# Optimization experiments

Measured on AMD Instinct MI355X. Metric: run time of the kernel, lower is better.

## Reference

```python
import jax, jax.numpy as jnp
import numpy as np
import math

C = 128

def setup_inputs() -> dict:
    key = jax.random.key(0)
    ks = jax.random.split(key, 6)
    B, N, M = 4, 8192, 2048
    s = 1.0 / math.sqrt(C)
    return {
        "pcd_up": jax.random.normal(ks[0], (B, C, N), dtype=jnp.float32),
        "pcd_down": jax.random.normal(ks[1], (B, C, M), dtype=jnp.float32),
        "wq": jax.random.normal(ks[2], (C, C), dtype=jnp.float32) * s,
        "wk": jax.random.normal(ks[3], (C, C), dtype=jnp.float32) * s,
        "wv": jax.random.normal(ks[4], (C, C), dtype=jnp.float32) * s,
        "wskip": jax.random.normal(ks[5], (C, C), dtype=jnp.float32) * s,
    }

def reference(pcd_up, pcd_down, wq, wk, wv, wskip):
    # Conv1d(kernel=1, no bias) == per-point linear: w @ x over channel dim
    q = jnp.einsum('oc,bcn->bon', wq, pcd_up)      # [B,C,N]
    k = jnp.einsum('oc,bcm->bom', wk, pcd_down)    # [B,C,M]
    v = jnp.einsum('oc,bcm->bom', wv, pcd_down)    # [B,C,M]
    energy = jnp.einsum('bcn,bcm->bnm', q, k)      # [B,N,M]
    scale = math.sqrt(q.shape[1])                  # sqrt(C): q.shape[-2] in torch
    attn = jax.nn.softmax(energy / scale, axis=-1)
    x = jnp.einsum('bnm,bcm->bcn', attn, v)        # [B,C,N]
    skip = jnp.einsum('oc,bcn->bon', wskip, pcd_up)
    return skip + x
```

## Files before the change

### kernel.cpp

```cpp
#include <hip/hip_runtime.h>
#include <hip/hip_bf16.h>
#include <math.h>

#define C_DIM 128
#define B_DIM 4
#define N_DIM 8192
#define M_DIM 2048
#define NT_KV 32

typedef unsigned short u16;
typedef unsigned int u32;
typedef short bf16x8 __attribute__((ext_vector_type(8)));
typedef float f32x4 __attribute__((ext_vector_type(4)));
typedef float f32x16 __attribute__((ext_vector_type(16)));
typedef u32 u32x4 __attribute__((ext_vector_type(4)));

__device__ inline u16 f2bf(float f) {
  u32 u = __builtin_bit_cast(u32, f);
  u += 0x7fffu + ((u >> 16) & 1u);
  return (u16)(u >> 16);
}
__device__ inline u32 cvtpk_bf16(float lo, float hi) {
  u32 r;
  asm("v_cvt_pk_bf16_f32 %0, %1, %2" : "=v"(r) : "v"(lo), "v"(hi));
  return r;
}

template <int MODE>
__device__ inline void proj_pass(const float* __restrict__ W, float wscale,
                                 const u16* __restrict__ xt_s,
                                 u16* __restrict__ outh,
                                 int b, int X, int x0, int t) {
  const int l = t & 63, w = t >> 6, lr = l & 15, lh = (l >> 4) & 3;
  bf16x8 wf[2][4];
  #pragma unroll
  for (int ot = 0; ot < 2; ++ot)
    #pragma unroll
    for (int kc = 0; kc < 4; ++kc) {
      const float* wp = &W[(size_t)(w * 32 + ot * 16 + lr) * 128 + kc * 32 + lh * 8];
      float4 a0 = *(const float4*)wp;
      float4 a1 = *(const float4*)(wp + 4);
      bf16x8 f;
      f[0] = (short)f2bf(a0.x * wscale); f[1] = (short)f2bf(a0.y * wscale);
      f[2] = (short)f2bf(a0.z * wscale); f[3] = (short)f2bf(a0.w * wscale);
      f[4] = (short)f2bf(a1.x * wscale); f[5] = (short)f2bf(a1.y * wscale);
      f[6] = (short)f2bf(a1.z * wscale); f[7] = (short)f2bf(a1.w * wscale);
      wf[ot][kc] = f;
    }
  f32x4 acc[2][4];
  #pragma unroll
  for (int ot = 0; ot < 2; ++ot)
    #pragma unroll
    for (int xt = 0; xt < 4; ++xt) acc[ot][xt] = 0.f;

  #pragma unroll
  for (int xt = 0; xt < 4; ++xt) {
    int xx = xt * 16 + lr;
    #pragma unroll
    for (int kc = 0; kc < 4; ++kc) {
      bf16x8 bf = *(const bf16x8*)&xt_s[xx * 128 + ((kc * 32 + lh * 8) ^ ((xx & 15) << 3))];
      #pragma unroll
      for (int ot = 0; ot < 2; ++ot)
        acc[ot][xt] = __builtin_amdgcn_mfma_f32_16x16x32_bf16(wf[ot][kc], bf, acc[ot][xt], 0, 0, 0);
    }
  }
  #pragma unroll
  for (int ot = 0; ot < 2; ++ot) {
    int o0 = w * 32 + ot * 16 + lh * 4;
    #pragma unroll
    for (int xt = 0; xt < 4; ++xt) {
      int xg = x0 + xt * 16 + lr;
      if constexpr (MODE == 0) {
        u16 h[4];
        #pragma unroll
        for (int r = 0; r < 4; ++r) h[r] = f2bf(acc[ot][xt][r]);
        *(uint2*)&outh[((size_t)b * X + xg) * 128 + o0] = *(uint2*)h;
      } else if constexpr (MODE == 2) {
        int tt = xg >> 6, mt = (xg >> 5) & 1, ms = xg & 31;
        int kcK = o0 >> 4, lh1p = (o0 >> 3) & 1, e0 = o0 & 7;
        u16 h[4];
        #pragma unroll
        for (int r = 0; r < 4; ++r) h[r] = f2bf(acc[ot][xt][r]);
        size_t off = ((((size_t)(b * NT_KV + tt) * 2 + mt) * 8 + kcK) * 64 + (ms | (lh1p << 5))) * 8 + e0;
        *(uint2*)&outh[off] = *(uint2*)h;
      } else {
        int tt = xg >> 6, sv = (xg >> 4) & 3, lh1m = (xg >> 3) & 1, e = xg & 7;
        int ctv = o0 >> 5;
        #pragma unroll
        for (int r = 0; r < 4; ++r) {
          int cs = (o0 + r) & 31;
          size_t off = ((((size_t)(b * NT_KV + tt) * 4 + ctv) * 4 + sv) * 64 + (cs | (lh1m << 5))) * 8 + e;
          outh[off] = f2bf(acc[ot][xt][r]);
        }
      }
    }
  }
}

__global__ __launch_bounds__(256, 2) void proj_all(
    const float* __restrict__ up, const float* __restrict__ down,
    const float* __restrict__ wq, const float* __restrict__ wk,
    const float* __restrict__ wv, u16* __restrict__ Qt,
    u16* __restrict__ Kt2, u16* __restrict__ Vp, float qscale) {
  __shared__ u16 xt_s[64 * 128];
  const int bid = blockIdx.x, t = threadIdx.x;
  const bool isQ = bid < 512;
  const int sub = isQ ? bid : bid - 512;
  const int b = sub & 3;
  const int x0 = (sub >> 2) * 64;
  const int X = isQ ? N_DIM : M_DIM;
  const float* in = isQ ? up : down;

  #pragma unroll
  for (int pp = 0; pp < 8; ++pp) {
    int c = pp * 16 + (t >> 4);
    int x4 = (t & 15) * 4;
    float4 v = *(const float4*)&in[((size_t)b * 128 + c) * X + x0 + x4];
    xt_s[(x4 + 0) * 128 + (c ^ (((x4 + 0) & 15) << 3))] = f2bf(v.x);
    xt_s[(x4 + 1) * 128 + (c ^ (((x4 + 1) & 15) << 3))] = f2bf(v.y);
    xt_s[(x4 + 2) * 128 + (c ^ (((x4 + 2) & 15) << 3))] = f2bf(v.z);
    xt_s[(x4 + 3) * 128 + (c ^ (((x4 + 3) & 15) << 3))] = f2bf(v.w);
  }
  __syncthreads();
  if (isQ) {
    proj_pass<0>(wq, qscale, xt_s, Qt, b, X, x0, t);
  } else {
    proj_pass<2>(wk, 1.0f, xt_s, Kt2, b, X, x0, t);
    proj_pass<3>(wv, 1.0f, xt_s, Vp, b, X, x0, t);
  }
}

__device__ inline void stage_kv(const u16* __restrict__ gK, const u16* __restrict__ gV,
                                u16* lK, u16* lV, int tile, int t) {
  const u16* ks = gK + (size_t)tile * 8192;
  const u16* vs = gV + (size_t)tile * 8192;
  #pragma unroll
  for (int i = 0; i < 2; ++i) {
    int ch = t + i * 512;
    __builtin_amdgcn_global_load_lds((const __attribute__((address_space(1))) void*)(ks + ch * 8),
                                     (__attribute__((address_space(3))) void*)(lK + ch * 8), 16, 0, 0);
    __builtin_amdgcn_global_load_lds((const __attribute__((address_space(1))) void*)(vs + ch * 8),
                                     (__attribute__((address_space(3))) void*)(lV + ch * 8), 16, 0, 0);
  }
}

__global__ __launch_bounds__(512, 2) void attn_kernel(
    const u16* __restrict__ Qt, const u16* __restrict__ Kt2,
    const u16* __restrict__ Vp, const float* __restrict__ up,
    const float* __restrict__ wskip, float* __restrict__ out) {
  __shared__ union {
    u16 kv[2][2][8192];
    float od[4][4096];
  } lds;
  __shared__ float lb[4][64];

  const int bid = blockIdx.x;
  const int xcd = bid & 7, b = xcd & 3, slot = bid >> 3;
  const int n0 = ((xcd >> 2) * 32 + slot) * 128;
  const int t = threadIdx.x, w = t >> 6, l = t & 63, lh1 = l >> 5;
  const int h = w >> 2;
  const int nq = n0 + (w & 3) * 32 + (l & 31);

  bf16x8 qf[8];
  #pragma unroll
  for (int kc = 0; kc < 8; ++kc)
    qf[kc] = *(const bf16x8*)&Qt[((size_t)b * N_DIM + nq) * 128 + kc * 16 + lh1 * 8];

  const u16* gK = Kt2 + (size_t)b * 262144;
  const u16* gV = Vp + (size_t)b * 262144;

  f32x16 acco[4];
  #pragma unroll
  for (int ct = 0; ct < 4; ++ct) acco[ct] = 0.f;
  float lrun = 0.f;

  bf16x8 pf[2];
  bf16x8 vreg[8];
  #pragma unroll
  for (int u = 0; u < 2; ++u) pf[u] = (bf16x8)0;
  #pragma unroll
  for (int x = 0; x < 8; ++x) vreg[x] = (bf16x8)0;

  stage_kv(gK, gV, lds.kv[0][0], lds.kv[0][1], 0, t);
  __syncthreads();

  #pragma unroll 2
  for (int i = 0; i < NT_KV; ++i) {
    const int cur = i & 1;
    if (i + 1 < NT_KV)
      stage_kv(gK, gV, lds.kv[cur ^ 1][0], lds.kv[cur ^ 1][1], i + 1, t);
    const u16* kl = lds.kv[cur][0];
    const u16* vl = lds.kv[cur][1];

    f32x16 sacc = 0.f;
    __builtin_amdgcn_s_setprio(1);
    #pragma unroll
    for (int kc = 0; kc < 8; ++kc) {
      bf16x8 kf = *(const bf16x8*)&kl[((h * 8 + kc) * 64 + l) * 8];
      sacc = __builtin_amdgcn_mfma_f32_32x32x16_bf16(kf, qf[kc], sacc, 0, 0, 0);
    }
    #pragma unroll
    for (int u = 0; u < 2; ++u)
      #pragma unroll
      for (int ct = 0; ct < 4; ++ct)
        acco[ct] = __builtin_amdgcn_mfma_f32_32x32x16_bf16(vreg[ct * 2 + u], pf[u], acco[ct], 0, 0, 0);
    __builtin_amdgcn_s_setprio(0);
    __builtin_amdgcn_sched_barrier(0);

    #pragma unroll
    for (int ct = 0; ct < 4; ++ct)
      #pragma unroll
      for (int u = 0; u < 2; ++u)
        vreg[ct * 2 + u] = *(const bf16x8*)&vl[((ct * 4 + 2 * h + u) * 64 + l) * 8];

    #pragma unroll
    for (int r = 0; r < 16; ++r) sacc[r] = exp2f(sacc[r]);
    {
      float a0 = (sacc[0] + sacc[1]) + (sacc[2] + sacc[3]);
      float a1 = (sacc[4] + sacc[5]) + (sacc[6] + sacc[7]);
      float a2 = (sacc[8] + sacc[9]) + (sacc[10] + sacc[11]);
      float a3 = (sacc[12] + sacc[13]) + (sacc[14] + sacc[15]);
      lrun += (a0 + a1) + (a2 + a3);
    }
    u32 gp[4][2];
    #pragma unroll
    for (int j = 0; j < 4; ++j) {
      gp[j][0] = cvtpk_bf16(sacc[j * 4 + 0], sacc[j * 4 + 1]);
      gp[j][1] = cvtpk_bf16(sacc[j * 4 + 2], sacc[j * 4 + 3]);
    }
    #pragma unroll
    for (int u = 0; u < 2; ++u) {
      u32 a0 = gp[2 * u][0], a1 = gp[2 * u][1];
      u32 b0 = gp[2 * u + 1][0], b1 = gp[2 * u + 1][1];
      asm("v_permlane32_swap_b32 %0, %1" : "+v"(a0), "+v"(b0));
      asm("v_permlane32_swap_b32 %0, %1" : "+v"(a1), "+v"(b1));
      u32x4 fv; fv.x = a0; fv.y = a1; fv.z = b0; fv.w = b1;
      pf[u] = __builtin_bit_cast(bf16x8, fv);
    }
    __syncthreads();
  }

  __builtin_amdgcn_s_setprio(1);
  #pragma unroll
  for (int u = 0; u < 2; ++u)
    #pragma unroll
    for (int ct = 0; ct < 4; ++ct)
      acco[ct] = __builtin_amdgcn_mfma_f32_32x32x16_bf16(vreg[ct * 2 + u], pf[u], acco[ct], 0, 0, 0);
  __builtin_amdgcn_s_setprio(0);

  float lt = lrun + __shfl_xor(lrun, 32, 64);

  if (w >= 4) {
    float* dst = lds.od[w - 4];
    #pragma unroll
    for (int ct = 0; ct < 4; ++ct)
      #pragma unroll
      for (int r = 0; r < 16; ++r) dst[(ct * 16 + r) * 64 + l] = acco[ct][r];
    lb[w - 4][l] = lt;
  }
  __syncthreads();
  if (w < 4) {
    const float* src = lds.od[w];
    #pragma unroll
    for (int ct = 0; ct < 4; ++ct)
      #pragma unroll
      for (int r = 0; r < 16; ++r) acco[ct][r] += src[(ct * 16 + r) * 64 + l];
    lt += lb[w][l];

    float inv = 1.0f / lt;
    #pragma unroll
    for (int ct = 0; ct < 4; ++ct)
      #pragma unroll
      for (int r = 0; r < 16; ++r) acco[ct][r] *= inv;

    const float* upb = up + (size_t)b * 128 * N_DIM;
    #pragma unroll
    for (int kc = 0; kc < 8; ++kc) {
      float uv[8];
      #pragma unroll
      for (int e = 0; e < 8; ++e)
        uv[e] = upb[(size_t)(kc * 16 + lh1 * 8 + e) * N_DIM + nq];
      u32x4 ufv;
      ufv.x = cvtpk_bf16(uv[0], uv[1]);
      ufv.y = cvtpk_bf16(uv[2], uv[3]);
      ufv.z = cvtpk_bf16(uv[4], uv[5]);
      ufv.w = cvtpk_bf16(uv[6], uv[7]);
      bf16x8 upf = __builtin_bit_cast(bf16x8, ufv);
      #pragma unroll
      for (int ct = 0; ct < 4; ++ct) {
        const float* wp = &wskip[(size_t)(ct * 32 + (l & 31)) * 128 + kc * 16 + lh1 * 8];
        float4 w0 = *(const float4*)wp;
        float4 w1 = *(const float4*)(wp + 4);
        u32x4 wfv;
        wfv.x = cvtpk_bf16(w0.x, w0.y);
        wfv.y = cvtpk_bf16(w0.z, w0.w);
        wfv.z = cvtpk_bf16(w1.x, w1.y);
        wfv.w = cvtpk_bf16(w1.z, w1.w);
        bf16x8 wsf = __builtin_bit_cast(bf16x8, wfv);
        acco[ct] = __builtin_amdgcn_mfma_f32_32x32x16_bf16(wsf, upf, acco[ct], 0, 0, 0);
      }
    }

    #pragma unroll
    for (int ct = 0; ct < 4; ++ct)
      #pragma unroll
      for (int r = 0; r < 16; ++r) {
        int c = ct * 32 + (r & 3) + 8 * (r >> 2) + 4 * lh1;
        out[((size_t)b * 128 + c) * N_DIM + nq] = acco[ct][r];
      }
  }
}

extern "C" void kernel_launch(void* const* d_in, const int* in_sizes, int n_in,
                              void* d_out, int out_size, void* d_ws, size_t ws_size,
                              hipStream_t stream) {
  const float* up    = (const float*)d_in[0];
  const float* down  = (const float*)d_in[1];
  const float* wq    = (const float*)d_in[2];
  const float* wk    = (const float*)d_in[3];
  const float* wv    = (const float*)d_in[4];
  const float* wskip = (const float*)d_in[5];
  float* out = (float*)d_out;

  u16* Qt  = (u16*)d_ws;
  u16* Kt2 = Qt + (size_t)B_DIM * N_DIM * C_DIM;
  u16* Vp  = Kt2 + (size_t)B_DIM * M_DIM * C_DIM;

  const float qscale = (float)(1.4426950408889634 / sqrt(128.0));

  hipLaunchKernelGGL((proj_all), dim3(640), dim3(256), 0, stream,
                     up, down, wq, wk, wv, Qt, Kt2, Vp, qscale);
  hipLaunchKernelGGL((attn_kernel), dim3(256), dim3(512), 0, stream,
                     Qt, Kt2, Vp, up, wskip, out);
}
```

Baseline: 70.34 us.

## Software-pipeline softmax of previous tile behind current QK MFMA

Restructures the KV loop so the QK^T MFMAs of tile i are issued first, then the exp2/sum/bf16-pack softmax of tile i-1 runs while those MFMAs are in flight, followed by the PV MFMAs. Two score accumulators (sA/sB) alternate, with a peeled prologue and epilogue. The goal is to overlap VALU exponentials with matrix-core work inside each wave. The cost is higher register pressure from the extra f32x16 accumulator, which could lower occupancy or cause spills.

After: 70.70 us. About the same (+0.5%).

```diff
diff --git a/kernel.cpp b/kernel.cpp
--- a/kernel.cpp
+++ b/kernel.cpp
@@ -176,29 +176,52 @@
 
   bf16x8 pf[2];
   bf16x8 vreg[8];
-  #pragma unroll
-  for (int u = 0; u < 2; ++u) pf[u] = (bf16x8)0;
-  #pragma unroll
-  for (int x = 0; x < 8; ++x) vreg[x] = (bf16x8)0;
-
-  stage_kv(gK, gV, lds.kv[0][0], lds.kv[0][1], 0, t);
-  __syncthreads();
-
-  #pragma unroll 2
-  for (int i = 0; i < NT_KV; ++i) {
+  f32x16 sA, sB;
+
+  auto do_sm = [&](f32x16& sp) {
+    #pragma unroll
+    for (int r = 0; r < 16; ++r) sp[r] = exp2f(sp[r]);
+    float a0 = (sp[0] + sp[1]) + (sp[2] + sp[3]);
+    float a1 = (sp[4] + sp[5]) + (sp[6] + sp[7]);
+    float a2 = (sp[8] + sp[9]) + (sp[10] + sp[11]);
+    float a3 = (sp[12] + sp[13]) + (sp[14] + sp[15]);
+    lrun += (a0 + a1) + (a2 + a3);
+    u32 gp[4][2];
+    #pragma unroll
+    for (int j = 0; j < 4; ++j) {
+      gp[j][0] = cvtpk_bf16(sp[j * 4 + 0], sp[j * 4 + 1]);
+      gp[j][1] = cvtpk_bf16(sp[j * 4 + 2], sp[j * 4 + 3]);
+    }
+    #pragma unroll
+    for (int u = 0; u < 2; ++u) {
+      u32 a0_ = gp[2 * u][0], a1_ = gp[2 * u][1];
+      u32 b0_ = gp[2 * u + 1][0], b1_ = gp[2 * u + 1][1];
+      asm("v_permlane32_swap_b32 %0, %1" : "+v"(a0_), "+v"(b0_));
+      asm("v_permlane32_swap_b32 %0, %1" : "+v"(a1_), "+v"(b1_));
+      u32x4 fv; fv.x = a0_; fv.y = a1_; fv.z = b0_; fv.w = b1_;
+      pf[u] = __builtin_bit_cast(bf16x8, fv);
+    }
+  };
+
+  auto body = [&](int i, f32x16& sc, f32x16& sp) {
     const int cur = i & 1;
     if (i + 1 < NT_KV)
       stage_kv(gK, gV, lds.kv[cur ^ 1][0], lds.kv[cur ^ 1][1], i + 1, t);
     const u16* kl = lds.kv[cur][0];
     const u16* vl = lds.kv[cur][1];
 
-    f32x16 sacc = 0.f;
+    sc = 0.f;
     __builtin_amdgcn_s_setprio(1);
     #pragma unroll
     for (int kc = 0; kc < 8; ++kc) {
       bf16x8 kf = *(const bf16x8*)&kl[((h * 8 + kc) * 64 + l) * 8];
-      sacc = __builtin_amdgcn_mfma_f32_32x32x16_bf16(kf, qf[kc], sacc, 0, 0, 0);
-    }
+      sc = __builtin_amdgcn_mfma_f32_32x32x16_bf16(kf, qf[kc], sc, 0, 0, 0);
+    }
+    __builtin_amdgcn_s_setprio(0);
+
+    do_sm(sp);
+
+    __builtin_amdgcn_s_setprio(1);
     #pragma unroll
     for (int u = 0; u < 2; ++u)
       #pragma unroll
@@ -213,33 +236,39 @@
       for (int u = 0; u < 2; ++u)
         vreg[ct * 2 + u] = *(const bf16x8*)&vl[((ct * 4 + 2 * h + u) * 64 + l) * 8];
 
-    #pragma unroll
-    for (int r = 0; r < 16; ++r) sacc[r] = exp2f(sacc[r]);
-    {
-      float a0 = (sacc[0] + sacc[1]) + (sacc[2] + sacc[3]);
-      float a1 = (sacc[4] + sacc[5]) + (sacc[6] + sacc[7]);
-      float a2 = (sacc[8] + sacc[9]) + (sacc[10] + sacc[11]);
-      float a3 = (sacc[12] + sacc[13]) + (sacc[14] + sacc[15]);
-      lrun += (a0 + a1) + (a2 + a3);
-    }
-    u32 gp[4][2];
-    #pragma unroll
-    for (int j = 0; j < 4; ++j) {
-      gp[j][0] = cvtpk_bf16(sacc[j * 4 + 0], sacc[j * 4 + 1]);
-      gp[j][1] = cvtpk_bf16(sacc[j * 4 + 2], sacc[j * 4 + 3]);
-    }
-    #pragma unroll
-    for (int u = 0; u < 2; ++u) {
-      u32 a0 = gp[2 * u][0], a1 = gp[2 * u][1];
-      u32 b0 = gp[2 * u + 1][0], b1 = gp[2 * u + 1][1];
-      asm("v_permlane32_swap_b32 %0, %1" : "+v"(a0), "+v"(b0));
-      asm("v_permlane32_swap_b32 %0, %1" : "+v"(a1), "+v"(b1));
-      u32x4 fv; fv.x = a0; fv.y = a1; fv.z = b0; fv.w = b1;
-      pf[u] = __builtin_bit_cast(bf16x8, fv);
-    }
     __syncthreads();
-  }
-
+  };
+
+  stage_kv(gK, gV, lds.kv[0][0], lds.kv[0][1], 0, t);
+  __syncthreads();
+
+  {
+    stage_kv(gK, gV, lds.kv[1][0], lds.kv[1][1], 1, t);
+    const u16* kl = lds.kv[0][0];
+    const u16* vl = lds.kv[0][1];
+    sA = 0.f;
+    __builtin_amdgcn_s_setprio(1);
+    #pragma unroll
+    for (int kc = 0; kc < 8; ++kc) {
+      bf16x8 kf = *(const bf16x8*)&kl[((h * 8 + kc) * 64 + l) * 8];
+      sA = __builtin_amdgcn_mfma_f32_32x32x16_bf16(kf, qf[kc], sA, 0, 0, 0);
+    }
+    __builtin_amdgcn_s_setprio(0);
+    #pragma unroll
+    for (int ct = 0; ct < 4; ++ct)
+      #pragma unroll
+      for (int u = 0; u < 2; ++u)
+        vreg[ct * 2 + u] = *(const bf16x8*)&vl[((ct * 4 + 2 * h + u) * 64 + l) * 8];
+    __syncthreads();
+  }
+
+  for (int ii = 0; ii < 15; ++ii) {
+    body(2 * ii + 1, sB, sA);
+    body(2 * ii + 2, sA, sB);
+  }
+  body(31, sB, sA);
+
+  do_sm(sB);
   __builtin_amdgcn_s_setprio(1);
   #pragma unroll
   for (int u = 0; u < 2; ++u)
```

## Double KV tile per iteration and give each warp two key subtiles

Applied to the files above, without the earlier changes.

Each loop iteration now stages a KV tile twice as large (16 iterations instead of 32). Each warp computes two 32x32 score subtiles and four PV MFMA steps per iteration, which halves the number of barriers and grows the MFMA work available for interleaving. The larger LDS buffers and register arrays force occupancy down from 2 to 1 block per CU (launch bounds changed). The sched_barrier between MFMA and softmax phases is removed, and the per-half-wave (h) key split is now done by LDS offset.

Result: slower. 74.32 us (+5.6%).

```diff
diff --git a/kernel.cpp b/kernel.cpp
--- a/kernel.cpp
+++ b/kernel.cpp
@@ -132,10 +132,10 @@
 
 __device__ inline void stage_kv(const u16* __restrict__ gK, const u16* __restrict__ gV,
                                 u16* lK, u16* lV, int tile, int t) {
-  const u16* ks = gK + (size_t)tile * 8192;
-  const u16* vs = gV + (size_t)tile * 8192;
-  #pragma unroll
-  for (int i = 0; i < 2; ++i) {
+  const u16* ks = gK + (size_t)tile * 16384;
+  const u16* vs = gV + (size_t)tile * 16384;
+  #pragma unroll
+  for (int i = 0; i < 4; ++i) {
     int ch = t + i * 512;
     __builtin_amdgcn_global_load_lds((const __attribute__((address_space(1))) void*)(ks + ch * 8),
                                      (__attribute__((address_space(3))) void*)(lK + ch * 8), 16, 0, 0);
@@ -144,12 +144,12 @@
   }
 }
 
-__global__ __launch_bounds__(512, 2) void attn_kernel(
+__global__ __launch_bounds__(512, 1) void attn_kernel(
     const u16* __restrict__ Qt, const u16* __restrict__ Kt2,
     const u16* __restrict__ Vp, const float* __restrict__ up,
     const float* __restrict__ wskip, float* __restrict__ out) {
   __shared__ union {
-    u16 kv[2][2][8192];
+    u16 kv[2][2][16384];
     float od[4][4096];
   } lds;
   __shared__ float lb[4][64];
@@ -174,78 +174,84 @@
   for (int ct = 0; ct < 4; ++ct) acco[ct] = 0.f;
   float lrun = 0.f;
 
-  bf16x8 pf[2];
-  bf16x8 vreg[8];
-  #pragma unroll
-  for (int u = 0; u < 2; ++u) pf[u] = (bf16x8)0;
-  #pragma unroll
-  for (int x = 0; x < 8; ++x) vreg[x] = (bf16x8)0;
+  bf16x8 pf[4];
+  bf16x8 vreg[16];
+  #pragma unroll
+  for (int s = 0; s < 4; ++s) pf[s] = (bf16x8)0;
+  #pragma unroll
+  for (int x = 0; x < 16; ++x) vreg[x] = (bf16x8)0;
 
   stage_kv(gK, gV, lds.kv[0][0], lds.kv[0][1], 0, t);
   __syncthreads();
 
-  #pragma unroll 2
-  for (int i = 0; i < NT_KV; ++i) {
+  for (int i = 0; i < 16; ++i) {
     const int cur = i & 1;
-    if (i + 1 < NT_KV)
+    if (i + 1 < 16)
       stage_kv(gK, gV, lds.kv[cur ^ 1][0], lds.kv[cur ^ 1][1], i + 1, t);
-    const u16* kl = lds.kv[cur][0];
-    const u16* vl = lds.kv[cur][1];
-
-    f32x16 sacc = 0.f;
+    const u16* kl = lds.kv[cur][0] + h * 8192;
+    const u16* vl = lds.kv[cur][1] + h * 8192;
+
+    f32x16 sacc[2];
+    sacc[0] = 0.f; sacc[1] = 0.f;
     __builtin_amdgcn_s_setprio(1);
     #pragma unroll
     for (int kc = 0; kc < 8; ++kc) {
-      bf16x8 kf = *(const bf16x8*)&kl[((h * 8 + kc) * 64 + l) * 8];
-      sacc = __builtin_amdgcn_mfma_f32_32x32x16_bf16(kf, qf[kc], sacc, 0, 0, 0);
-    }
-    #pragma unroll
-    for (int u = 0; u < 2; ++u)
+      #pragma unroll
+      for (int mt = 0; mt < 2; ++mt) {
+        bf16x8 kf = *(const bf16x8*)&kl[((mt * 8 + kc) * 64 + l) * 8];
+        sacc[mt] = __builtin_amdgcn_mfma_f32_32x32x16_bf16(kf, qf[kc], sacc[mt], 0, 0, 0);
+      }
+    }
+    #pragma unroll
+    for (int s = 0; s < 4; ++s)
       #pragma unroll
       for (int ct = 0; ct < 4; ++ct)
-        acco[ct] = __builtin_amdgcn_mfma_f32_32x32x16_bf16(vreg[ct * 2 + u], pf[u], acco[ct], 0, 0, 0);
+        acco[ct] = __builtin_amdgcn_mfma_f32_32x32x16_bf16(vreg[ct * 4 + s], pf[s], acco[ct], 0, 0, 0);
     __builtin_amdgcn_s_setprio(0);
-    __builtin_amdgcn_sched_barrier(0);
-
-    #pragma unroll
-    for (int ct = 0; ct < 4; ++ct)
-      #pragma unroll
-      for (int u = 0; u < 2; ++u)
-        vreg[ct * 2 + u] = *(const bf16x8*)&vl[((ct * 4 + 2 * h + u) * 64 + l) * 8];
-
-    #pragma unroll
-    for (int r = 0; r < 16; ++r) sacc[r] = exp2f(sacc[r]);
-    {
-      float a0 = (sacc[0] + sacc[1]) + (sacc[2] + sacc[3]);
-      float a1 = (sacc[4] + sacc[5]) + (sacc[6] + sacc[7]);
-      float a2 = (sacc[8] + sacc[9]) + (sacc[10] + sacc[11]);
-      float a3 = (sacc[12] + sacc[13]) + (sacc[14] + sacc[15]);
+
+    #pragma unroll
+    for (int ct = 0; ct < 4; ++ct)
+      #pragma unroll
+      for (int s = 0; s < 4; ++s)
+        vreg[ct * 4 + s] = *(const bf16x8*)&vl[((ct * 4 + s) * 64 + l) * 8];
+
+    #pragma unroll
+    for (int mt = 0; mt < 2; ++mt) {
+      #pragma unroll
+      for (int r = 0; r < 16; ++r) sacc[mt][r] = exp2f(sacc[mt][r]);
+      float a0 = (sacc[mt][0] + sacc[mt][1]) + (sacc[mt][2] + sacc[mt][3]);
+      float a1 = (sacc[mt][4] + sacc[mt][5]) + (sacc[mt][6] + sacc[mt][7]);
+      float a2 = (sacc[mt][8] + sacc[mt][9]) + (sacc[mt][10] + sacc[mt][11]);
+      float a3 = (sacc[mt][12] + sacc[mt][13]) + (sacc[mt][14] + sacc[mt][15]);
       lrun += (a0 + a1) + (a2 + a3);
     }
-    u32 gp[4][2];
-    #pragma unroll
-    for (int j = 0; j < 4; ++j) {
-      gp[j][0] = cvtpk_bf16(sacc[j * 4 + 0], sacc[j * 4 + 1]);
-      gp[j][1] = cvtpk_bf16(sacc[j * 4 + 2], sacc[j * 4 + 3]);
-    }
-    #pragma unroll
-    for (int u = 0; u < 2; ++u) {
-      u32 a0 = gp[2 * u][0], a1 = gp[2 * u][1];
-      u32 b0 = gp[2 * u + 1][0], b1 = gp[2 * u + 1][1];
-      asm("v_permlane32_swap_b32 %0, %1" : "+v"(a0), "+v"(b0));
-      asm("v_permlane32_swap_b32 %0, %1" : "+v"(a1), "+v"(b1));
-      u32x4 fv; fv.x = a0; fv.y = a1; fv.z = b0; fv.w = b1;
-      pf[u] = __builtin_bit_cast(bf16x8, fv);
+    #pragma unroll
+    for (int mt = 0; mt < 2; ++mt) {
+      u32 gp[4][2];
+      #pragma unroll
+      for (int j = 0; j < 4; ++j) {
+        gp[j][0] = cvtpk_bf16(sacc[mt][j * 4 + 0], sacc[mt][j * 4 + 1]);
+        gp[j][1] = cvtpk_bf16(sacc[mt][j * 4 + 2], sacc[mt][j * 4 + 3]);
+      }
+      #pragma unroll
+      for (int u = 0; u < 2; ++u) {
+        u32 a0 = gp[2 * u][0], a1 = gp[2 * u][1];
+        u32 b0 = gp[2 * u + 1][0], b1 = gp[2 * u + 1][1];
+        asm("v_permlane32_swap_b32 %0, %1" : "+v"(a0), "+v"(b0));
+        asm("v_permlane32_swap_b32 %0, %1" : "+v"(a1), "+v"(b1));
+        u32x4 fv; fv.x = a0; fv.y = a1; fv.z = b0; fv.w = b1;
+        pf[mt * 2 + u] = __builtin_bit_cast(bf16x8, fv);
+      }
     }
     __syncthreads();
   }
 
   __builtin_amdgcn_s_setprio(1);
   #pragma unroll
-  for (int u = 0; u < 2; ++u)
-    #pragma unroll
-    for (int ct = 0; ct < 4; ++ct)
-      acco[ct] = __builtin_amdgcn_mfma_f32_32x32x16_bf16(vreg[ct * 2 + u], pf[u], acco[ct], 0, 0, 0);
+  for (int s = 0; s < 4; ++s)
+    #pragma unroll
+    for (int ct = 0; ct < 4; ++ct)
+      acco[ct] = __builtin_amdgcn_mfma_f32_32x32x16_bf16(vreg[ct * 4 + s], pf[s], acco[ct], 0, 0, 0);
   __builtin_amdgcn_s_setprio(0);
 
   float lt = lrun + __shfl_xor(lrun, 32, 64);
```
